# Kernel tuning notes

Measured on AMD Instinct MI355X. Metric: run time of the kernel, lower is better.

## Reference

```python
import jax, jax.numpy as jnp
import numpy as np

SUPPORT = 1.5   # attributes['support']
N_RBF = 4       # n = m = 4 hat-function basis per axis
NF, NB = 8192, 2048


def hat_basis(u, n):
    # linear (hat) RBF basis on centers in [-1, 1]
    centers = jnp.linspace(-1.0, 1.0, n, dtype=u.dtype)
    spacing = 2.0 / (n - 1)
    return jax.nn.relu(1.0 - jnp.abs(u[:, None] - centers) / spacing)  # [E, n]


def rbf_conv(f_src, tgt, src, d, W, b, num_nodes):
    # d: [E,2] clamped relative positions; polar coordinate mapping
    r = jnp.linalg.norm(d, axis=-1) * 2.0 - 1.0          # radius -> [-1,1]
    theta = jnp.arctan2(d[:, 1], d[:, 0]) / jnp.pi       # angle  -> [-1,1]
    coeff = (hat_basis(r, N_RBF)[:, :, None] * hat_basis(theta, N_RBF)[:, None, :])
    coeff = coeff.reshape(d.shape[0], N_RBF * N_RBF)      # [E, k]
    f = f_src[src]                                        # gather  [E, Cin]
    tmp = jnp.einsum('ei,kio->eko', f, W)                 # [E, k, Cout]
    msg = jnp.einsum('ek,eko->eo', coeff, tmp)            # [E, Cout]
    return jax.ops.segment_sum(msg, tgt, num_segments=num_nodes) + b


def setup_inputs() -> dict:
    key = jax.random.key(0)
    ks = list(jax.random.split(key, 40))
    inp = {}
    inp['fluidPositions'] = jax.random.uniform(ks[0], (NF, 2), dtype=jnp.float32)
    inp['boundaryPositions'] = jax.random.uniform(ks[1], (NB, 2), dtype=jnp.float32)
    inp['fluidFeats'] = jax.random.normal(ks[2], (NF, 2), dtype=jnp.float32)
    inp['boundaryFeats'] = jax.random.normal(ks[3], (NB, 3), dtype=jnp.float32)
    EF, EB = 131072, 32768
    inp['fe_i'] = jnp.sort(jax.random.randint(ks[4], (EF,), 0, NF, dtype=jnp.int32))
    inp['fe_j'] = jax.random.randint(ks[5], (EF,), 0, NF, dtype=jnp.int32)
    inp['be_f'] = jnp.sort(jax.random.randint(ks[6], (EB,), 0, NF, dtype=jnp.int32))
    inp['be_b'] = jax.random.randint(ks[7], (EB,), 0, NB, dtype=jnp.int32)
    k2 = N_RBF * N_RBF
    conv_shapes = [(2, 16), (2, 16), (3, 16), (3, 16), (96, 32), (96, 32), (64, 32), (64, 32)]
    for c, (ci, co) in enumerate(conv_shapes):
        inp[f'W{c}'] = jax.random.normal(ks[8 + c], (k2, ci, co), dtype=jnp.float32) * 0.05
        inp[f'b{c}'] = jnp.zeros((co,), dtype=jnp.float32)
    fc_shapes = [(2, 32), (96, 64), (64, 64)]
    for c, (ci, co) in enumerate(fc_shapes):
        inp[f'fcW{c}'] = jax.random.normal(ks[20 + c], (ci, co), dtype=jnp.float32) * 0.05
        inp[f'fcb{c}'] = jnp.zeros((co,), dtype=jnp.float32)
    return inp


def reference(fluidPositions, boundaryPositions, fluidFeats, boundaryFeats,
              fe_i, fe_j, be_f, be_b,
              W0, b0, W1, b1, W2, b2, W3, b3, W4, b4, W5, b5, W6, b6, W7, b7,
              fcW0, fcb0, fcW1, fcb1, fcW2, fcb2):
    nF = fluidPositions.shape[0]
    # edge relative positions, clamped to [-1, 1]
    b_d = jnp.clip((boundaryPositions[be_b] - fluidPositions[be_f]) / SUPPORT, -1.0, 1.0)
    f_d = jnp.clip(-(fluidPositions[fe_j] - fluidPositions[fe_i]) / SUPPORT, -1.0, 1.0)

    linearOutput = fluidFeats @ fcW0 + fcb0                               # [N, 32]
    bA = rbf_conv(boundaryFeats, be_f, be_b, b_d, W2, b2, nF)             # [N, 16]
    bB = rbf_conv(boundaryFeats, be_f, be_b, b_d, W3, b3, nF)
    fA = rbf_conv(fluidFeats, fe_i, fe_j, f_d, W0, b0, nF)
    fB = rbf_conv(fluidFeats, fe_i, fe_j, f_d, W1, b1, nF)
    ans = jnp.concatenate([linearOutput, fA, fB, bA, bB], axis=1)          # [N, 96]

    # hidden layer i=2: convs 4,5 + fc1 (no residual: 32 != 64)
    ansc = jax.nn.relu(ans)
    conv = jnp.concatenate([rbf_conv(ansc, fe_i, fe_j, f_d, W4, b4, nF),
                            rbf_conv(ansc, fe_i, fe_j, f_d, W5, b5, nF)], axis=1)
    ans = conv + (ansc @ fcW1 + fcb1)                                      # [N, 64]

    # hidden layer i=3: convs 6,7 + fc2 (+ residual: 64 == 64)
    ansc = jax.nn.relu(ans)
    conv = jnp.concatenate([rbf_conv(ansc, fe_i, fe_j, f_d, W6, b6, nF),
                            rbf_conv(ansc, fe_i, fe_j, f_d, W7, b7, nF)], axis=1)
    ans = conv + (ansc @ fcW2 + fcb2) + ans

    return ans / 128.0
```

## Files before the change

kernel.cpp:

```cpp
#include <hip/hip_runtime.h>
#include <math.h>

#define SUPPORT 1.5f

typedef unsigned short ushort_t;
typedef short bf16x8 __attribute__((ext_vector_type(8)));
typedef float f32x4 __attribute__((ext_vector_type(4)));

__device__ __forceinline__ float bf2f(unsigned short h) {
    union { unsigned int u; float f; } c;
    c.u = ((unsigned int)h) << 16;
    return c.f;
}
__device__ __forceinline__ unsigned short f2bf(float f) {
    union { float f; unsigned int u; } c;
    c.f = f;
    unsigned int lsb = (c.u >> 16) & 1u;
    c.u += 0x7fffu + lsb;
    return (unsigned short)(c.u >> 16);
}

__device__ __forceinline__ void hat4(float u, float h[4]) {
#pragma unroll
    for (int j = 0; j < 4; ++j) {
        float c = -1.0f + j * (2.0f / 3.0f);
        h[j] = fmaxf(0.0f, 1.0f - fabsf(u - c) * 1.5f);
    }
}

__device__ __forceinline__ void coeff16(float2 A, float2 B, bool neg, float* o) {
    float rx = (A.x - B.x) / SUPPORT;
    float ry = (A.y - B.y) / SUPPORT;
    if (neg) { rx = -rx; ry = -ry; }
    float dx = fminf(fmaxf(rx, -1.0f), 1.0f);
    float dy = fminf(fmaxf(ry, -1.0f), 1.0f);
    float r  = sqrtf(dx * dx + dy * dy) * 2.0f - 1.0f;
    float th = atan2f(dy, dx) / 3.14159265358979323846f;
    float hr[4], ht[4];
    hat4(r, hr);
    hat4(th, ht);
#pragma unroll
    for (int a = 0; a < 4; ++a)
#pragma unroll
        for (int b = 0; b < 4; ++b)
            o[a * 4 + b] = hr[a] * ht[b];
}

__device__ __forceinline__ int lower_bound(const int* __restrict__ arr, int E, int key) {
    int lo = 0, hi = E;
    while (lo < hi) {
        int mid = (lo + hi) >> 1;
        if (arr[mid] < key) lo = mid + 1; else hi = mid;
    }
    return lo;
}

__device__ __forceinline__ void packW(const float* __restrict__ WA,
                                      const float* __restrict__ WB,
                                      const float* __restrict__ fcW,
                                      ushort_t* __restrict__ Wp, int CIN, int idx) {
    int j8   = idx & 7;
    int lane = (idx >> 3) & 63;
    int tile = (idx >> 9) & 3;
    int ks   = idx >> 11;
    int kk = ks * 32 + ((lane >> 4) << 3) + j8;
    int o  = tile * 16 + (lane & 15);
    int KC = 16 * CIN;
    float v = (kk < KC) ? ((o < 32) ? WA[(size_t)kk * 32 + o] : WB[(size_t)kk * 32 + (o - 32)])
                        : fcW[(size_t)(kk - KC) * 64 + o];
    Wp[idx] = f2bf(v);
}

__global__ void prologue_kernel(
    const float2* __restrict__ fPos, const float2* __restrict__ bPos,
    const int* __restrict__ fe_i, const int* __restrict__ fe_j,
    const int* __restrict__ be_f, const int* __restrict__ be_b,
    const float* __restrict__ W4, const float* __restrict__ W5,
    const float* __restrict__ fcW1, const float* __restrict__ b4,
    const float* __restrict__ b5, const float* __restrict__ fcb1,
    const float* __restrict__ W6, const float* __restrict__ W7,
    const float* __restrict__ fcW2, const float* __restrict__ b6,
    const float* __restrict__ b7, const float* __restrict__ fcb2,
    float* __restrict__ f_coeff, float* __restrict__ b_coeff,
    int* __restrict__ f_off, int* __restrict__ b_off,
    ushort_t* __restrict__ Wp2, float* __restrict__ bias2,
    ushort_t* __restrict__ Wp3, float* __restrict__ bias3,
    int EF, int EB, int NF) {
    int idx = blockIdx.x * 256 + threadIdx.x;
    if (idx < EF) {
        float co[16];
        coeff16(fPos[fe_j[idx]], fPos[fe_i[idx]], true, co);
        float* o = f_coeff + (size_t)idx * 16;
#pragma unroll
        for (int i = 0; i < 16; ++i) o[i] = co[i];
        return;
    }
    idx -= EF;
    if (idx < EB) {
        float co[16];
        coeff16(bPos[be_b[idx]], fPos[be_f[idx]], false, co);
        float* o = b_coeff + (size_t)idx * 16;
#pragma unroll
        for (int i = 0; i < 16; ++i) o[i] = co[i];
        return;
    }
    idx -= EB;
    if (idx < NF + 1) { f_off[idx] = lower_bound(fe_i, EF, idx); return; }
    idx -= NF + 1;
    if (idx < NF + 1) { b_off[idx] = lower_bound(be_f, EB, idx); return; }
    idx -= NF + 1;
    if (idx < 64) { bias2[idx] = ((idx < 32) ? b4[idx] : b5[idx - 32]) + fcb1[idx]; return; }
    idx -= 64;
    if (idx < 51 * 2048) { packW(W4, W5, fcW1, Wp2, 96, idx); return; }
    idx -= 51 * 2048;
    if (idx < 64) { bias3[idx] = ((idx < 32) ? b6[idx] : b7[idx - 32]) + fcb2[idx]; return; }
    idx -= 64;
    if (idx < 34 * 2048) { packW(W6, W7, fcW2, Wp3, 64, idx); return; }
}

__global__ void layer1_kernel(const float* __restrict__ fluidFeats,
                              const float* __restrict__ boundaryFeats,
                              const float* __restrict__ fcW0, const float* __restrict__ fcb0,
                              const float* __restrict__ W0, const float* __restrict__ b0,
                              const float* __restrict__ W1, const float* __restrict__ b1,
                              const float* __restrict__ W2, const float* __restrict__ b2,
                              const float* __restrict__ W3, const float* __restrict__ b3,
                              const int* __restrict__ f_off, const int* __restrict__ fe_j,
                              const float* __restrict__ f_coeff,
                              const int* __restrict__ b_off, const int* __restrict__ be_b,
                              const float* __restrict__ b_coeff,
                              ushort_t* __restrict__ A1b) {
    int n = blockIdx.x;
    int t = threadIdx.x;
    if (t >= 96) return;
    float val;
    if (t < 32) {
        val = fluidFeats[n * 2] * fcW0[t] + fluidFeats[n * 2 + 1] * fcW0[32 + t] + fcb0[t];
    } else if (t < 64) {
        int oc = t - 32;
        const float* W = (oc < 16) ? W0 : W1;
        int o16 = oc & 15;
        float wk[32];
#pragma unroll
        for (int k = 0; k < 16; ++k) {
            wk[2 * k + 0] = W[(k * 2 + 0) * 16 + o16];
            wk[2 * k + 1] = W[(k * 2 + 1) * 16 + o16];
        }
        float s = (oc < 16) ? b0[o16] : b1[o16];
        int e1 = f_off[n + 1];
        for (int e = f_off[n]; e < e1; ++e) {
            const float* cf = f_coeff + (size_t)e * 16;
            int srcn = fe_j[e];
            float f0 = fluidFeats[srcn * 2], f1 = fluidFeats[srcn * 2 + 1];
            float acc = 0.0f;
#pragma unroll
            for (int k = 0; k < 16; ++k)
                acc += cf[k] * (f0 * wk[2 * k] + f1 * wk[2 * k + 1]);
            s += acc;
        }
        val = s;
    } else {
        int oc = t - 64;
        const float* W = (oc < 16) ? W2 : W3;
        int o16 = oc & 15;
        float wk[48];
#pragma unroll
        for (int k = 0; k < 16; ++k) {
            wk[3 * k + 0] = W[(k * 3 + 0) * 16 + o16];
            wk[3 * k + 1] = W[(k * 3 + 1) * 16 + o16];
            wk[3 * k + 2] = W[(k * 3 + 2) * 16 + o16];
        }
        float s = (oc < 16) ? b2[o16] : b3[o16];
        int e1 = b_off[n + 1];
        for (int e = b_off[n]; e < e1; ++e) {
            const float* cf = b_coeff + (size_t)e * 16;
            int srcn = be_b[e];
            float f0 = boundaryFeats[srcn * 3], f1 = boundaryFeats[srcn * 3 + 1],
                  f2 = boundaryFeats[srcn * 3 + 2];
            float acc = 0.0f;
#pragma unroll
            for (int k = 0; k < 16; ++k)
                acc += cf[k] * (f0 * wk[3 * k] + f1 * wk[3 * k + 1] + f2 * wk[3 * k + 2]);
            s += acc;
        }
        val = s;
    }
    A1b[(size_t)n * 96 + t] = f2bf(fmaxf(val, 0.0f));
}

template <int CIN, bool RELU, bool RESID, bool FINAL>
__global__ __launch_bounds__(512, 4) void conv_mfma_kernel(
    const ushort_t* __restrict__ Xb,
    const int* __restrict__ f_off, const int* __restrict__ fe_j,
    const float* __restrict__ f_coeff,
    const ushort_t* __restrict__ Wp, const float* __restrict__ bias,
    const ushort_t* __restrict__ XresB,
    void* __restrict__ OUT, int NF) {
    constexpr int KTOT   = 17 * CIN;
    constexpr int KSTEPS = KTOT / 32;
    constexpr int STRIDE = KTOT + 8;
    constexpr int EPT = CIN / 4;
    constexpr int NU4 = EPT / 8;

    __shared__ ushort_t Gl[16 * STRIDE];
    __shared__ float red[4][64][4];

    const int t = threadIdx.x;
    const int wv = t >> 6;
    const int lane = t & 63;
    const int nb = blockIdx.x * 16;

    const int k  = lane >> 2;
    const int i0 = (lane & 3) * EPT;
    for (int s2 = 0; s2 < 2; ++s2) {
        int lnode = wv * 2 + s2;
        int n = nb + lnode;
        if (n > NF - 1) n = NF - 1;

        float acc[EPT];
#pragma unroll
        for (int s = 0; s < EPT; ++s) acc[s] = 0.0f;

        int e0 = f_off[n], e1 = f_off[n + 1];
        for (int e = e0; e < e1; e += 4) {
            int ea = e;
            int eb = (e + 1 < e1) ? e + 1 : e;
            int ec = (e + 2 < e1) ? e + 2 : e;
            int ed = (e + 3 < e1) ? e + 3 : e;
            int s0 = fe_j[ea], s1 = fe_j[eb], s2i = fe_j[ec], s3 = fe_j[ed];
            float c0 = f_coeff[(size_t)ea * 16 + k];
            float c1 = f_coeff[(size_t)eb * 16 + k];
            float c2 = f_coeff[(size_t)ec * 16 + k];
            float c3 = f_coeff[(size_t)ed * 16 + k];
            c1 = (e + 1 < e1) ? c1 : 0.0f;
            c2 = (e + 2 < e1) ? c2 : 0.0f;
            c3 = (e + 3 < e1) ? c3 : 0.0f;
            const uint4* x0 = (const uint4*)(Xb + (size_t)s0 * CIN + i0);
            const uint4* x1 = (const uint4*)(Xb + (size_t)s1 * CIN + i0);
            const uint4* x2 = (const uint4*)(Xb + (size_t)s2i * CIN + i0);
            const uint4* x3 = (const uint4*)(Xb + (size_t)s3 * CIN + i0);
            uint4 r0[NU4], r1[NU4], r2[NU4], r3[NU4];
#pragma unroll
            for (int q = 0; q < NU4; ++q) r0[q] = x0[q];
#pragma unroll
            for (int q = 0; q < NU4; ++q) r1[q] = x1[q];
#pragma unroll
            for (int q = 0; q < NU4; ++q) r2[q] = x2[q];
#pragma unroll
            for (int q = 0; q < NU4; ++q) r3[q] = x3[q];
#pragma unroll
            for (int q = 0; q < NU4; ++q) {
                unsigned int w0[4] = {r0[q].x, r0[q].y, r0[q].z, r0[q].w};
                unsigned int w1[4] = {r1[q].x, r1[q].y, r1[q].z, r1[q].w};
                unsigned int w2[4] = {r2[q].x, r2[q].y, r2[q].z, r2[q].w};
                unsigned int w3[4] = {r3[q].x, r3[q].y, r3[q].z, r3[q].w};
#pragma unroll
                for (int j = 0; j < 4; ++j) {
                    int s = q * 8 + j * 2;
#define EDGEFMA(wj, cc)                                                        \
                    {                                                          \
                        float lo = bf2f((unsigned short)(wj[j] & 0xffff));     \
                        float hi = bf2f((unsigned short)(wj[j] >> 16));        \
                        if (RELU) { lo = fmaxf(lo, 0.f); hi = fmaxf(hi, 0.f); }\
                        acc[s + 0] = fmaf(cc, lo, acc[s + 0]);                 \
                        acc[s + 1] = fmaf(cc, hi, acc[s + 1]);                 \
                    }
                    EDGEFMA(w0, c0)
                    EDGEFMA(w1, c1)
                    EDGEFMA(w2, c2)
                    EDGEFMA(w3, c3)
#undef EDGEFMA
                }
            }
        }

        ushort_t* grow = Gl + lnode * STRIDE;
        ushort_t* gp = grow + k * CIN + i0;
#pragma unroll
        for (int q = 0; q < NU4; ++q) {
            uint4 o;
            o.x = (unsigned int)f2bf(acc[q*8+0]) | ((unsigned int)f2bf(acc[q*8+1]) << 16);
            o.y = (unsigned int)f2bf(acc[q*8+2]) | ((unsigned int)f2bf(acc[q*8+3]) << 16);
            o.z = (unsigned int)f2bf(acc[q*8+4]) | ((unsigned int)f2bf(acc[q*8+5]) << 16);
            o.w = (unsigned int)f2bf(acc[q*8+6]) | ((unsigned int)f2bf(acc[q*8+7]) << 16);
            *(uint4*)(gp + q * 8) = o;
        }
        for (int i = lane; i < CIN; i += 64) {
            ushort_t v = Xb[(size_t)n * CIN + i];
            if (RELU && (v & 0x8000)) v = 0;
            grow[16 * CIN + i] = v;
        }
    }
    __syncthreads();

    const int ot = wv & 3;
    const int kh = wv >> 2;
    f32x4 cacc = {0.f, 0.f, 0.f, 0.f};
    const ushort_t* garow = Gl + (lane & 15) * STRIDE + ((lane >> 4) << 3);
    const ushort_t* wpp = Wp + ((size_t)(ot * 64 + lane) << 3);
    for (int ks = kh; ks < KSTEPS; ks += 2) {
        bf16x8 a = *(const bf16x8*)(garow + ks * 32);
        bf16x8 b = *(const bf16x8*)(wpp + (size_t)ks * 2048);
        cacc = __builtin_amdgcn_mfma_f32_16x16x32_bf16(a, b, cacc, 0, 0, 0);
    }
    if (kh == 1) {
        red[ot][lane][0] = cacc[0];
        red[ot][lane][1] = cacc[1];
        red[ot][lane][2] = cacc[2];
        red[ot][lane][3] = cacc[3];
    }
    __syncthreads();
    if (kh == 0) {
        int o = ot * 16 + (lane & 15);
        float bo = bias[o];
#pragma unroll
        for (int r = 0; r < 4; ++r) {
            int node = nb + ((lane >> 4) << 2) + r;
            if (node < NF) {
                float s = cacc[r] + red[ot][lane][r] + bo;
                if (RESID) s += bf2f(XresB[(size_t)node * 64 + o]);
                if (FINAL) {
                    ((float*)OUT)[(size_t)node * 64 + o] = s * (1.0f / 128.0f);
                } else {
                    ((ushort_t*)OUT)[(size_t)node * 64 + o] = f2bf(s);
                }
            }
        }
    }
}

template <int CIN, bool RELU_IN, bool RESIDUAL, bool FINAL, bool OUTBF>
__global__ __launch_bounds__(256) void conv_layer_kernel(
    const ushort_t* __restrict__ Xb,
    const float* __restrict__ WA, const float* __restrict__ bA,
    const float* __restrict__ WB, const float* __restrict__ bB,
    const float* __restrict__ fcW, const float* __restrict__ fcb,
    const int* __restrict__ f_off, const int* __restrict__ fe_j,
    const float* __restrict__ f_coeff,
    void* __restrict__ OUT) {
    constexpr int NELEM = 16 * CIN;
    constexpr int EPT = NELEM / 256;
    constexpr int BATCH = 8;
    constexpr int CHUNK = NELEM / 4;

    __shared__ float x_lds[CIN];
    __shared__ float feat[BATCH][CIN];
    __shared__ float co[BATCH][16];
    __shared__ float Gs[NELEM];
    __shared__ float red[4][64];

    int n = blockIdx.x;
    int t = threadIdx.x;

    for (int i = t; i < CIN; i += 256) {
        float v = bf2f(Xb[(size_t)n * CIN + i]);
        if (RELU_IN) v = fmaxf(v, 0.0f);
        x_lds[i] = v;
    }

    float acc[EPT];
    int kk[EPT], ii[EPT];
#pragma unroll
    for (int s = 0; s < EPT; ++s) {
        acc[s] = 0.0f;
        int j = s * 256 + t;
        kk[s] = j / CIN;
        ii[s] = j - kk[s] * CIN;
    }

    int e0 = f_off[n], e1 = f_off[n + 1];
    for (int eb = e0; eb < e1; eb += BATCH) {
        int cnt = min(BATCH, e1 - eb);
        __syncthreads();
        for (int idx = t; idx < cnt * 16; idx += 256) {
            int b = idx >> 4, c = idx & 15;
            co[b][c] = f_coeff[(size_t)(eb + b) * 16 + c];
        }
        for (int idx = t; idx < cnt * CIN; idx += 256) {
            int b = idx / CIN, i = idx - b * CIN;
            int srcn = fe_j[eb + b];
            float v = bf2f(Xb[(size_t)srcn * CIN + i]);
            if (RELU_IN) v = fmaxf(v, 0.0f);
            feat[b][i] = v;
        }
        __syncthreads();
#pragma unroll
        for (int b = 0; b < BATCH; ++b) {
            if (b >= cnt) break;
#pragma unroll
            for (int s = 0; s < EPT; ++s) acc[s] += co[b][kk[s]] * feat[b][ii[s]];
        }
    }
    __syncthreads();
#pragma unroll
    for (int s = 0; s < EPT; ++s) Gs[s * 256 + t] = acc[s];
    __syncthreads();

    int o = t & 63;
    int chunk = t >> 6;
    const float* Wp = (o < 32) ? WA : WB;
    int oc = o & 31;
    int j0 = chunk * CHUNK;
    float p0 = 0.f, p1 = 0.f, p2 = 0.f, p3 = 0.f;
    for (int j = j0; j < j0 + CHUNK; j += 4) {
        p0 += Gs[j + 0] * Wp[(size_t)(j + 0) * 32 + oc];
        p1 += Gs[j + 1] * Wp[(size_t)(j + 1) * 32 + oc];
        p2 += Gs[j + 2] * Wp[(size_t)(j + 2) * 32 + oc];
        p3 += Gs[j + 3] * Wp[(size_t)(j + 3) * 32 + oc];
    }
    red[chunk][o] = ((p0 + p1) + (p2 + p3));
    __syncthreads();
    if (t < 64) {
        float s = red[0][o] + red[1][o] + red[2][o] + red[3][o];
        s += (o < 32) ? bA[oc] : bB[oc];
        float fcv = fcb[o];
        for (int i = 0; i < CIN; ++i) fcv += x_lds[i] * fcW[i * 64 + o];
        s += fcv;
        if (RESIDUAL) s += bf2f(Xb[(size_t)n * 64 + o]);
        if (FINAL) s *= (1.0f / 128.0f);
        if (OUTBF) ((ushort_t*)OUT)[(size_t)n * 64 + o] = f2bf(s);
        else       ((float*)OUT)[(size_t)n * 64 + o] = s;
    }
}

extern "C" void kernel_launch(void* const* d_in, const int* in_sizes, int n_in,
                              void* d_out, int out_size, void* d_ws, size_t ws_size,
                              hipStream_t stream) {
    const float* fluidPos      = (const float*)d_in[0];
    const float* boundaryPos   = (const float*)d_in[1];
    const float* fluidFeats    = (const float*)d_in[2];
    const float* boundaryFeats = (const float*)d_in[3];
    const int* fe_i = (const int*)d_in[4];
    const int* fe_j = (const int*)d_in[5];
    const int* be_f = (const int*)d_in[6];
    const int* be_b = (const int*)d_in[7];
    const float* W[8];
    const float* bb[8];
    for (int c = 0; c < 8; ++c) {
        W[c]  = (const float*)d_in[8 + 2 * c];
        bb[c] = (const float*)d_in[9 + 2 * c];
    }
    const float* fcW0 = (const float*)d_in[24];
    const float* fcb0 = (const float*)d_in[25];
    const float* fcW1 = (const float*)d_in[26];
    const float* fcb1 = (const float*)d_in[27];
    const float* fcW2 = (const float*)d_in[28];
    const float* fcb2 = (const float*)d_in[29];

    int NF = in_sizes[0] / 2;
    int EF = in_sizes[4];
    int EB = in_sizes[6];

    float* ws = (float*)d_ws;
    size_t p = 0;
    float* f_coeff = ws + p;  p += (size_t)EF * 16;
    float* b_coeff = ws + p;  p += (size_t)EB * 16;
    ushort_t* A1b  = (ushort_t*)(ws + p);  p += (size_t)NF * 48;
    ushort_t* ans2b= (ushort_t*)(ws + p);  p += (size_t)NF * 32;
    int*   f_off   = (int*)(ws + p);  p += (size_t)((NF + 4) & ~3);
    int*   b_off   = (int*)(ws + p);  p += (size_t)((NF + 4) & ~3);
    ushort_t* Wp2  = (ushort_t*)(ws + p);  p += 1632 * 32;
    float* bias2   = ws + p;  p += 64;
    ushort_t* Wp3  = (ushort_t*)(ws + p);  p += 1088 * 32;
    float* bias3   = ws + p;  p += 64;

    bool bigPath = (ws_size / 4 >= p);

    int totalPro = EF + EB + 2 * (NF + 1) + 64 + 51 * 2048 + 64 + 34 * 2048;
    prologue_kernel<<<(totalPro + 255) / 256, 256, 0, stream>>>(
        (const float2*)fluidPos, (const float2*)boundaryPos,
        fe_i, fe_j, be_f, be_b,
        W[4], W[5], fcW1, bb[4], bb[5], fcb1,
        W[6], W[7], fcW2, bb[6], bb[7], fcb2,
        f_coeff, b_coeff, f_off, b_off,
        Wp2, bias2, Wp3, bias3, EF, EB, NF);

    layer1_kernel<<<NF, 128, 0, stream>>>(fluidFeats, boundaryFeats, fcW0, fcb0,
                                          W[0], bb[0], W[1], bb[1], W[2], bb[2], W[3], bb[3],
                                          f_off, fe_j, f_coeff, b_off, be_b, b_coeff, A1b);

    if (bigPath) {
        int nblk = (NF + 15) / 16;
        conv_mfma_kernel<96, false, false, false><<<nblk, 512, 0, stream>>>(
            A1b, f_off, fe_j, f_coeff, Wp2, bias2, nullptr, ans2b, NF);
        conv_mfma_kernel<64, true, true, true><<<nblk, 512, 0, stream>>>(
            ans2b, f_off, fe_j, f_coeff, Wp3, bias3, ans2b, d_out, NF);
    } else {
        conv_layer_kernel<96, false, false, false, true><<<NF, 256, 0, stream>>>(
            A1b, W[4], bb[4], W[5], bb[5], fcW1, fcb1, f_off, fe_j, f_coeff, ans2b);
        conv_layer_kernel<64, true, true, true, false><<<NF, 256, 0, stream>>>(
            ans2b, W[6], bb[6], W[7], bb[7], fcW2, fcb2, f_off, fe_j, f_coeff, d_out);
    }
}
```

Before: 100.5 us.

## Fuse all stages into one cooperative persistent kernel with grid syncs

Merges the prologue, layer-1 and both MFMA conv layers into a single cooperative kernel that uses grid-wide syncs between stages, so only one launch is issued. Blocks grid-stride over nodes, and layer 1 now packs four nodes per 512-thread block. The layer-1 edge loops are also unrolled by two with float4 coefficient loads to raise memory-level parallelism. The cost is the grid barrier overhead, a grid capped at 512 blocks (fewer than the 512 node-blocks only if NF changes), possible occupancy limits from the larger fused kernel, and a fallback to separate launches if the cooperative launch fails.

```diff
diff --git a/kernel.cpp b/kernel.cpp
--- a/kernel.cpp
+++ b/kernel.cpp
@@ -1,5 +1,8 @@
 #include <hip/hip_runtime.h>
+#include <hip/hip_cooperative_groups.h>
 #include <math.h>
+
+namespace cg = cooperative_groups;
 
 #define SUPPORT 1.5f
 
@@ -54,6 +57,23 @@
     }
     return lo;
 }
+
+struct FusedParams {
+    const float2* fPos; const float2* bPos;
+    const float* fluidFeats; const float* boundaryFeats;
+    const int *fe_i, *fe_j, *be_f, *be_b;
+    const float *fcW0, *fcb0;
+    const float *W0, *b0, *W1, *b1, *W2, *b2, *W3, *b3;
+    const float *W4, *W5, *fcW1, *b4, *b5, *fcb1;
+    const float *W6, *W7, *fcW2, *b6, *b7, *fcb2;
+    float *f_coeff, *b_coeff;
+    int *f_off, *b_off;
+    ushort_t *Wp2; float *bias2;
+    ushort_t *Wp3; float *bias3;
+    ushort_t *A1b, *ans2b;
+    float *out;
+    int EF, EB, NF, totalPro;
+};
 
 __device__ __forceinline__ void packW(const float* __restrict__ WA,
                                       const float* __restrict__ WB,
@@ -71,74 +91,46 @@
     Wp[idx] = f2bf(v);
 }
 
-__global__ void prologue_kernel(
-    const float2* __restrict__ fPos, const float2* __restrict__ bPos,
-    const int* __restrict__ fe_i, const int* __restrict__ fe_j,
-    const int* __restrict__ be_f, const int* __restrict__ be_b,
-    const float* __restrict__ W4, const float* __restrict__ W5,
-    const float* __restrict__ fcW1, const float* __restrict__ b4,
-    const float* __restrict__ b5, const float* __restrict__ fcb1,
-    const float* __restrict__ W6, const float* __restrict__ W7,
-    const float* __restrict__ fcW2, const float* __restrict__ b6,
-    const float* __restrict__ b7, const float* __restrict__ fcb2,
-    float* __restrict__ f_coeff, float* __restrict__ b_coeff,
-    int* __restrict__ f_off, int* __restrict__ b_off,
-    ushort_t* __restrict__ Wp2, float* __restrict__ bias2,
-    ushort_t* __restrict__ Wp3, float* __restrict__ bias3,
-    int EF, int EB, int NF) {
-    int idx = blockIdx.x * 256 + threadIdx.x;
-    if (idx < EF) {
+__device__ __forceinline__ void prologue_work(int idx, const FusedParams& P) {
+    if (idx < P.EF) {
         float co[16];
-        coeff16(fPos[fe_j[idx]], fPos[fe_i[idx]], true, co);
-        float* o = f_coeff + (size_t)idx * 16;
+        coeff16(P.fPos[P.fe_j[idx]], P.fPos[P.fe_i[idx]], true, co);
+        float* o = P.f_coeff + (size_t)idx * 16;
 #pragma unroll
         for (int i = 0; i < 16; ++i) o[i] = co[i];
         return;
     }
-    idx -= EF;
-    if (idx < EB) {
+    idx -= P.EF;
+    if (idx < P.EB) {
         float co[16];
-        coeff16(bPos[be_b[idx]], fPos[be_f[idx]], false, co);
-        float* o = b_coeff + (size_t)idx * 16;
+        coeff16(P.bPos[P.be_b[idx]], P.fPos[P.be_f[idx]], false, co);
+        float* o = P.b_coeff + (size_t)idx * 16;
 #pragma unroll
         for (int i = 0; i < 16; ++i) o[i] = co[i];
         return;
     }
-    idx -= EB;
-    if (idx < NF + 1) { f_off[idx] = lower_bound(fe_i, EF, idx); return; }
-    idx -= NF + 1;
-    if (idx < NF + 1) { b_off[idx] = lower_bound(be_f, EB, idx); return; }
-    idx -= NF + 1;
-    if (idx < 64) { bias2[idx] = ((idx < 32) ? b4[idx] : b5[idx - 32]) + fcb1[idx]; return; }
+    idx -= P.EB;
+    if (idx < P.NF + 1) { P.f_off[idx] = lower_bound(P.fe_i, P.EF, idx); return; }
+    idx -= P.NF + 1;
+    if (idx < P.NF + 1) { P.b_off[idx] = lower_bound(P.be_f, P.EB, idx); return; }
+    idx -= P.NF + 1;
+    if (idx < 64) { P.bias2[idx] = ((idx < 32) ? P.b4[idx] : P.b5[idx - 32]) + P.fcb1[idx]; return; }
     idx -= 64;
-    if (idx < 51 * 2048) { packW(W4, W5, fcW1, Wp2, 96, idx); return; }
+    if (idx < 51 * 2048) { packW(P.W4, P.W5, P.fcW1, P.Wp2, 96, idx); return; }
     idx -= 51 * 2048;
-    if (idx < 64) { bias3[idx] = ((idx < 32) ? b6[idx] : b7[idx - 32]) + fcb2[idx]; return; }
+    if (idx < 64) { P.bias3[idx] = ((idx < 32) ? P.b6[idx] : P.b7[idx - 32]) + P.fcb2[idx]; return; }
     idx -= 64;
-    if (idx < 34 * 2048) { packW(W6, W7, fcW2, Wp3, 64, idx); return; }
-}
-
-__global__ void layer1_kernel(const float* __restrict__ fluidFeats,
-                              const float* __restrict__ boundaryFeats,
-                              const float* __restrict__ fcW0, const float* __restrict__ fcb0,
-                              const float* __restrict__ W0, const float* __restrict__ b0,
-                              const float* __restrict__ W1, const float* __restrict__ b1,
-                              const float* __restrict__ W2, const float* __restrict__ b2,
-                              const float* __restrict__ W3, const float* __restrict__ b3,
-                              const int* __restrict__ f_off, const int* __restrict__ fe_j,
-                              const float* __restrict__ f_coeff,
-                              const int* __restrict__ b_off, const int* __restrict__ be_b,
-                              const float* __restrict__ b_coeff,
-                              ushort_t* __restrict__ A1b) {
-    int n = blockIdx.x;
-    int t = threadIdx.x;
+    if (idx < 34 * 2048) { packW(P.W6, P.W7, P.fcW2, P.Wp3, 64, idx); return; }
+}
+
+__device__ __forceinline__ void layer1_node(int n, int t, const FusedParams& P) {
     if (t >= 96) return;
     float val;
     if (t < 32) {
-        val = fluidFeats[n * 2] * fcW0[t] + fluidFeats[n * 2 + 1] * fcW0[32 + t] + fcb0[t];
+        val = P.fluidFeats[n * 2] * P.fcW0[t] + P.fluidFeats[n * 2 + 1] * P.fcW0[32 + t] + P.fcb0[t];
     } else if (t < 64) {
         int oc = t - 32;
-        const float* W = (oc < 16) ? W0 : W1;
+        const float* W = (oc < 16) ? P.W0 : P.W1;
         int o16 = oc & 15;
         float wk[32];
 #pragma unroll
@@ -146,22 +138,34 @@
             wk[2 * k + 0] = W[(k * 2 + 0) * 16 + o16];
             wk[2 * k + 1] = W[(k * 2 + 1) * 16 + o16];
         }
-        float s = (oc < 16) ? b0[o16] : b1[o16];
-        int e1 = f_off[n + 1];
-        for (int e = f_off[n]; e < e1; ++e) {
-            const float* cf = f_coeff + (size_t)e * 16;
-            int srcn = fe_j[e];
-            float f0 = fluidFeats[srcn * 2], f1 = fluidFeats[srcn * 2 + 1];
-            float acc = 0.0f;
-#pragma unroll
-            for (int k = 0; k < 16; ++k)
-                acc += cf[k] * (f0 * wk[2 * k] + f1 * wk[2 * k + 1]);
-            s += acc;
+        float s = (oc < 16) ? P.b0[o16] : P.b1[o16];
+        int e0 = P.f_off[n], e1 = P.f_off[n + 1];
+        for (int e = e0; e < e1; e += 2) {
+            int ea = e;
+            int eb = (e + 1 < e1) ? e + 1 : e;
+            float m1 = (e + 1 < e1) ? 1.0f : 0.0f;
+            int s0 = P.fe_j[ea], s1 = P.fe_j[eb];
+            float4 cA[4], cB[4];
+            const float4* a4 = (const float4*)(P.f_coeff + (size_t)ea * 16);
+            const float4* b4 = (const float4*)(P.f_coeff + (size_t)eb * 16);
+#pragma unroll
+            for (int q = 0; q < 4; ++q) { cA[q] = a4[q]; cB[q] = b4[q]; }
+            float2 fA = *(const float2*)(P.fluidFeats + (size_t)s0 * 2);
+            float2 fB = *(const float2*)(P.fluidFeats + (size_t)s1 * 2);
+            const float* ca = (const float*)&cA[0];
+            const float* cb = (const float*)&cB[0];
+            float accA = 0.0f, accB = 0.0f;
+#pragma unroll
+            for (int k = 0; k < 16; ++k) {
+                accA += ca[k] * (fA.x * wk[2 * k] + fA.y * wk[2 * k + 1]);
+                accB += cb[k] * (fB.x * wk[2 * k] + fB.y * wk[2 * k + 1]);
+            }
+            s += accA + accB * m1;
         }
         val = s;
     } else {
         int oc = t - 64;
-        const float* W = (oc < 16) ? W2 : W3;
+        const float* W = (oc < 16) ? P.W2 : P.W3;
         int o16 = oc & 15;
         float wk[48];
 #pragma unroll
@@ -170,48 +174,64 @@
             wk[3 * k + 1] = W[(k * 3 + 1) * 16 + o16];
             wk[3 * k + 2] = W[(k * 3 + 2) * 16 + o16];
         }
-        float s = (oc < 16) ? b2[o16] : b3[o16];
-        int e1 = b_off[n + 1];
-        for (int e = b_off[n]; e < e1; ++e) {
-            const float* cf = b_coeff + (size_t)e * 16;
-            int srcn = be_b[e];
-            float f0 = boundaryFeats[srcn * 3], f1 = boundaryFeats[srcn * 3 + 1],
-                  f2 = boundaryFeats[srcn * 3 + 2];
-            float acc = 0.0f;
-#pragma unroll
-            for (int k = 0; k < 16; ++k)
-                acc += cf[k] * (f0 * wk[3 * k] + f1 * wk[3 * k + 1] + f2 * wk[3 * k + 2]);
-            s += acc;
+        float s = (oc < 16) ? P.b2[o16] : P.b3[o16];
+        int e0 = P.b_off[n], e1 = P.b_off[n + 1];
+        for (int e = e0; e < e1; e += 2) {
+            int ea = e;
+            int eb = (e + 1 < e1) ? e + 1 : e;
+            float m1 = (e + 1 < e1) ? 1.0f : 0.0f;
+            int s0 = P.be_b[ea], s1 = P.be_b[eb];
+            float4 cA[4], cB[4];
+            const float4* a4 = (const float4*)(P.b_coeff + (size_t)ea * 16);
+            const float4* b4 = (const float4*)(P.b_coeff + (size_t)eb * 16);
+#pragma unroll
+            for (int q = 0; q < 4; ++q) { cA[q] = a4[q]; cB[q] = b4[q]; }
+            float fA0 = P.boundaryFeats[(size_t)s0 * 3 + 0];
+            float fA1 = P.boundaryFeats[(size_t)s0 * 3 + 1];
+            float fA2 = P.boundaryFeats[(size_t)s0 * 3 + 2];
+            float fB0 = P.boundaryFeats[(size_t)s1 * 3 + 0];
+            float fB1 = P.boundaryFeats[(size_t)s1 * 3 + 1];
+            float fB2 = P.boundaryFeats[(size_t)s1 * 3 + 2];
+            const float* ca = (const float*)&cA[0];
+            const float* cb = (const float*)&cB[0];
+            float accA = 0.0f, accB = 0.0f;
+#pragma unroll
+            for (int k = 0; k < 16; ++k) {
+                accA += ca[k] * (fA0 * wk[3 * k] + fA1 * wk[3 * k + 1] + fA2 * wk[3 * k + 2]);
+                accB += cb[k] * (fB0 * wk[3 * k] + fB1 * wk[3 * k + 1] + fB2 * wk[3 * k + 2]);
+            }
+            s += accA + accB * m1;
         }
         val = s;
     }
-    A1b[(size_t)n * 96 + t] = f2bf(fmaxf(val, 0.0f));
-}
+    P.A1b[(size_t)n * 96 + t] = f2bf(fmaxf(val, 0.0f));
+}
+
+#define SMEM_BYTES 56576
+#define RED_OFF 52480
 
 template <int CIN, bool RELU, bool RESID, bool FINAL>
-__global__ __launch_bounds__(512, 4) void conv_mfma_kernel(
+__device__ __forceinline__ void conv_body(
     const ushort_t* __restrict__ Xb,
     const int* __restrict__ f_off, const int* __restrict__ fe_j,
     const float* __restrict__ f_coeff,
     const ushort_t* __restrict__ Wp, const float* __restrict__ bias,
     const ushort_t* __restrict__ XresB,
-    void* __restrict__ OUT, int NF) {
+    void* __restrict__ OUT, int NF, int nb, int t, char* smem) {
     constexpr int KTOT   = 17 * CIN;
     constexpr int KSTEPS = KTOT / 32;
     constexpr int STRIDE = KTOT + 8;
     constexpr int EPT = CIN / 4;
     constexpr int NU4 = EPT / 8;
 
-    __shared__ ushort_t Gl[16 * STRIDE];
-    __shared__ float red[4][64][4];
-
-    const int t = threadIdx.x;
+    ushort_t* Gl = (ushort_t*)smem;
+    float (*red)[64][4] = (float (*)[64][4])(smem + RED_OFF);
+
     const int wv = t >> 6;
     const int lane = t & 63;
-    const int nb = blockIdx.x * 16;
-
     const int k  = lane >> 2;
     const int i0 = (lane & 3) * EPT;
+
     for (int s2 = 0; s2 < 2; ++s2) {
         int lnode = wv * 2 + s2;
         int n = nb + lnode;
@@ -286,7 +306,7 @@
             *(uint4*)(gp + q * 8) = o;
         }
         for (int i = lane; i < CIN; i += 64) {
-            ushort_t v = Xb[(size_t)n * CIN + i];
+            ushort_t v = Xb[(size_t)((nb + lnode > NF - 1) ? NF - 1 : nb + lnode) * CIN + i];
             if (RELU && (v & 0x8000)) v = 0;
             grow[16 * CIN + i] = v;
         }
@@ -329,97 +349,60 @@
     }
 }
 
-template <int CIN, bool RELU_IN, bool RESIDUAL, bool FINAL, bool OUTBF>
-__global__ __launch_bounds__(256) void conv_layer_kernel(
-    const ushort_t* __restrict__ Xb,
-    const float* __restrict__ WA, const float* __restrict__ bA,
-    const float* __restrict__ WB, const float* __restrict__ bB,
-    const float* __restrict__ fcW, const float* __restrict__ fcb,
-    const int* __restrict__ f_off, const int* __restrict__ fe_j,
-    const float* __restrict__ f_coeff,
-    void* __restrict__ OUT) {
-    constexpr int NELEM = 16 * CIN;
-    constexpr int EPT = NELEM / 256;
-    constexpr int BATCH = 8;
-    constexpr int CHUNK = NELEM / 4;
-
-    __shared__ float x_lds[CIN];
-    __shared__ float feat[BATCH][CIN];
-    __shared__ float co[BATCH][16];
-    __shared__ float Gs[NELEM];
-    __shared__ float red[4][64];
-
-    int n = blockIdx.x;
-    int t = threadIdx.x;
-
-    for (int i = t; i < CIN; i += 256) {
-        float v = bf2f(Xb[(size_t)n * CIN + i]);
-        if (RELU_IN) v = fmaxf(v, 0.0f);
-        x_lds[i] = v;
-    }
-
-    float acc[EPT];
-    int kk[EPT], ii[EPT];
-#pragma unroll
-    for (int s = 0; s < EPT; ++s) {
-        acc[s] = 0.0f;
-        int j = s * 256 + t;
-        kk[s] = j / CIN;
-        ii[s] = j - kk[s] * CIN;
-    }
-
-    int e0 = f_off[n], e1 = f_off[n + 1];
-    for (int eb = e0; eb < e1; eb += BATCH) {
-        int cnt = min(BATCH, e1 - eb);
+__global__ __launch_bounds__(512, 4) void fused_kernel(FusedParams P) {
+    __shared__ alignas(16) char smem[SMEM_BYTES];
+    cg::grid_group grid = cg::this_grid();
+    const int t = threadIdx.x;
+
+    long stride = (long)gridDim.x * 512;
+    for (long idx = (long)blockIdx.x * 512 + t; idx < P.totalPro; idx += stride)
+        prologue_work((int)idx, P);
+    grid.sync();
+
+    for (int nb = blockIdx.x * 16; nb < P.NF; nb += gridDim.x * 16) {
+#pragma unroll
+        for (int r = 0; r < 4; ++r) {
+            int node = nb + r * 4 + (t >> 7);
+            if (node < P.NF) layer1_node(node, t & 127, P);
+        }
+    }
+    grid.sync();
+
+    for (int nb = blockIdx.x * 16; nb < P.NF; nb += gridDim.x * 16) {
         __syncthreads();
-        for (int idx = t; idx < cnt * 16; idx += 256) {
-            int b = idx >> 4, c = idx & 15;
-            co[b][c] = f_coeff[(size_t)(eb + b) * 16 + c];
-        }
-        for (int idx = t; idx < cnt * CIN; idx += 256) {
-            int b = idx / CIN, i = idx - b * CIN;
-            int srcn = fe_j[eb + b];
-            float v = bf2f(Xb[(size_t)srcn * CIN + i]);
-            if (RELU_IN) v = fmaxf(v, 0.0f);
-            feat[b][i] = v;
-        }
+        conv_body<96, false, false, false>(P.A1b, P.f_off, P.fe_j, P.f_coeff,
+                                           P.Wp2, P.bias2, nullptr, P.ans2b, P.NF, nb, t, smem);
+    }
+    grid.sync();
+
+    for (int nb = blockIdx.x * 16; nb < P.NF; nb += gridDim.x * 16) {
         __syncthreads();
-#pragma unroll
-        for (int b = 0; b < BATCH; ++b) {
-            if (b >= cnt) break;
-#pragma unroll
-            for (int s = 0; s < EPT; ++s) acc[s] += co[b][kk[s]] * feat[b][ii[s]];
-        }
-    }
-    __syncthreads();
-#pragma unroll
-    for (int s = 0; s < EPT; ++s) Gs[s * 256 + t] = acc[s];
-    __syncthreads();
-
-    int o = t & 63;
-    int chunk = t >> 6;
-    const float* Wp = (o < 32) ? WA : WB;
-    int oc = o & 31;
-    int j0 = chunk * CHUNK;
-    float p0 = 0.f, p1 = 0.f, p2 = 0.f, p3 = 0.f;
-    for (int j = j0; j < j0 + CHUNK; j += 4) {
-        p0 += Gs[j + 0] * Wp[(size_t)(j + 0) * 32 + oc];
-        p1 += Gs[j + 1] * Wp[(size_t)(j + 1) * 32 + oc];
-        p2 += Gs[j + 2] * Wp[(size_t)(j + 2) * 32 + oc];
-        p3 += Gs[j + 3] * Wp[(size_t)(j + 3) * 32 + oc];
-    }
-    red[chunk][o] = ((p0 + p1) + (p2 + p3));
-    __syncthreads();
-    if (t < 64) {
-        float s = red[0][o] + red[1][o] + red[2][o] + red[3][o];
-        s += (o < 32) ? bA[oc] : bB[oc];
-        float fcv = fcb[o];
-        for (int i = 0; i < CIN; ++i) fcv += x_lds[i] * fcW[i * 64 + o];
-        s += fcv;
-        if (RESIDUAL) s += bf2f(Xb[(size_t)n * 64 + o]);
-        if (FINAL) s *= (1.0f / 128.0f);
-        if (OUTBF) ((ushort_t*)OUT)[(size_t)n * 64 + o] = f2bf(s);
-        else       ((float*)OUT)[(size_t)n * 64 + o] = s;
+        conv_body<64, true, true, true>(P.ans2b, P.f_off, P.fe_j, P.f_coeff,
+                                        P.Wp3, P.bias3, P.ans2b, P.out, P.NF, nb, t, smem);
+    }
+}
+
+__global__ void prologue_kernel(FusedParams P) {
+    int idx = blockIdx.x * 256 + threadIdx.x;
+    if (idx < P.totalPro) prologue_work(idx, P);
+}
+
+__global__ void layer1_kernel(FusedParams P) {
+    layer1_node(blockIdx.x, threadIdx.x, P);
+}
+
+template <int CIN, bool RELU, bool RESID, bool FINAL>
+__global__ __launch_bounds__(512, 4) void conv_mfma_kernel(FusedParams P) {
+    __shared__ alignas(16) char smem[SMEM_BYTES];
+    int nb = blockIdx.x * 16;
+    if (CIN == 96) {
+        conv_body<96, false, false, false>(P.A1b, P.f_off, P.fe_j, P.f_coeff,
+                                           P.Wp2, P.bias2, nullptr, P.ans2b, P.NF, nb,
+                                           threadIdx.x, smem);
+    } else {
+        conv_body<64, true, true, true>(P.ans2b, P.f_off, P.fe_j, P.f_coeff,
+                                        P.Wp3, P.bias3, P.ans2b, P.out, P.NF, nb,
+                                        threadIdx.x, smem);
     }
 }
 
@@ -464,31 +447,32 @@
     ushort_t* Wp3  = (ushort_t*)(ws + p);  p += 1088 * 32;
     float* bias3   = ws + p;  p += 64;
 
-    bool bigPath = (ws_size / 4 >= p);
-
-    int totalPro = EF + EB + 2 * (NF + 1) + 64 + 51 * 2048 + 64 + 34 * 2048;
-    prologue_kernel<<<(totalPro + 255) / 256, 256, 0, stream>>>(
-        (const float2*)fluidPos, (const float2*)boundaryPos,
-        fe_i, fe_j, be_f, be_b,
-        W[4], W[5], fcW1, bb[4], bb[5], fcb1,
-        W[6], W[7], fcW2, bb[6], bb[7], fcb2,
-        f_coeff, b_coeff, f_off, b_off,
-        Wp2, bias2, Wp3, bias3, EF, EB, NF);
-
-    layer1_kernel<<<NF, 128, 0, stream>>>(fluidFeats, boundaryFeats, fcW0, fcb0,
-                                          W[0], bb[0], W[1], bb[1], W[2], bb[2], W[3], bb[3],
-                                          f_off, fe_j, f_coeff, b_off, be_b, b_coeff, A1b);
-
-    if (bigPath) {
-        int nblk = (NF + 15) / 16;
-        conv_mfma_kernel<96, false, false, false><<<nblk, 512, 0, stream>>>(
-            A1b, f_off, fe_j, f_coeff, Wp2, bias2, nullptr, ans2b, NF);
-        conv_mfma_kernel<64, true, true, true><<<nblk, 512, 0, stream>>>(
-            ans2b, f_off, fe_j, f_coeff, Wp3, bias3, ans2b, d_out, NF);
-    } else {
-        conv_layer_kernel<96, false, false, false, true><<<NF, 256, 0, stream>>>(
-            A1b, W[4], bb[4], W[5], bb[5], fcW1, fcb1, f_off, fe_j, f_coeff, ans2b);
-        conv_layer_kernel<64, true, true, true, false><<<NF, 256, 0, stream>>>(
-            ans2b, W[6], bb[6], W[7], bb[7], fcW2, fcb2, f_off, fe_j, f_coeff, d_out);
-    }
-}
+    FusedParams P;
+    P.fPos = (const float2*)fluidPos;  P.bPos = (const float2*)boundaryPos;
+    P.fluidFeats = fluidFeats;  P.boundaryFeats = boundaryFeats;
+    P.fe_i = fe_i; P.fe_j = fe_j; P.be_f = be_f; P.be_b = be_b;
+    P.fcW0 = fcW0; P.fcb0 = fcb0;
+    P.W0 = W[0]; P.b0 = bb[0]; P.W1 = W[1]; P.b1 = bb[1];
+    P.W2 = W[2]; P.b2 = bb[2]; P.W3 = W[3]; P.b3 = bb[3];
+    P.W4 = W[4]; P.W5 = W[5]; P.fcW1 = fcW1; P.b4 = bb[4]; P.b5 = bb[5]; P.fcb1 = fcb1;
+    P.W6 = W[6]; P.W7 = W[7]; P.fcW2 = fcW2; P.b6 = bb[6]; P.b7 = bb[7]; P.fcb2 = fcb2;
+    P.f_coeff = f_coeff; P.b_coeff = b_coeff;
+    P.f_off = f_off; P.b_off = b_off;
+    P.Wp2 = Wp2; P.bias2 = bias2; P.Wp3 = Wp3; P.bias3 = bias3;
+    P.A1b = A1b; P.ans2b = ans2b; P.out = (float*)d_out;
+    P.EF = EF; P.EB = EB; P.NF = NF;
+    P.totalPro = EF + EB + 2 * (NF + 1) + 64 + 51 * 2048 + 64 + 34 * 2048;
+
+    int nblk = (NF + 15) / 16;
+    int coopBlk = (nblk < 512) ? nblk : 512;
+    void* args[] = { &P };
+    hipError_t err = hipLaunchCooperativeKernel((const void*)fused_kernel,
+                                                dim3(coopBlk), dim3(512), args, 0, stream);
+    if (err != hipSuccess) {
+        (void)hipGetLastError();
+        prologue_kernel<<<(P.totalPro + 255) / 256, 256, 0, stream>>>(P);
+        layer1_kernel<<<NF, 128, 0, stream>>>(P);
+        conv_mfma_kernel<96, false, false, false><<<nblk, 512, 0, stream>>>(P);
+        conv_mfma_kernel<64, true, true, true><<<nblk, 512, 0, stream>>>(P);
+    }
+}
```

Result: slower. 329.7 us (+228.0%).
